# Kernel tuning notes

Measured on AMD Instinct MI355X. Metric: run time of the kernel, lower is better.

## Reference

```python
import jax, jax.numpy as jnp
import numpy as np

D_MODEL = 2048
N_HEADS = 16
HEAD_DIM = D_MODEL // N_HEADS
D_FF = 4 * D_MODEL
BATCH = 2
SEQ = 2048
LN_EPS = 1e-5


def setup_inputs() -> dict:
    key = jax.random.key(0)
    ks = jax.random.split(key, 12)
    s = 0.02
    return {
        "x": jax.random.normal(ks[0], (BATCH, SEQ, D_MODEL), dtype=jnp.float32),
        "alibi_bias": jax.random.normal(ks[1], (N_HEADS, SEQ, SEQ), dtype=jnp.float32),
        "W_q": jax.random.normal(ks[2], (D_MODEL, D_MODEL), dtype=jnp.float32) * s,
        "W_k": jax.random.normal(ks[3], (D_MODEL, D_MODEL), dtype=jnp.float32) * s,
        "W_v": jax.random.normal(ks[4], (D_MODEL, D_MODEL), dtype=jnp.float32) * s,
        "W_o": jax.random.normal(ks[5], (D_MODEL, D_MODEL), dtype=jnp.float32) * s,
        "ln1_g": jnp.ones((D_MODEL,), dtype=jnp.float32),
        "ln1_b": jnp.zeros((D_MODEL,), dtype=jnp.float32),
        "ln2_g": jnp.ones((D_MODEL,), dtype=jnp.float32),
        "ln2_b": jnp.zeros((D_MODEL,), dtype=jnp.float32),
        "ffn_w1": jax.random.normal(ks[6], (D_MODEL, D_FF), dtype=jnp.float32) * s,
        "ffn_b1": jnp.zeros((D_FF,), dtype=jnp.float32),
        "ffn_w2": jax.random.normal(ks[7], (D_FF, D_MODEL), dtype=jnp.float32) * s,
        "ffn_b2": jnp.zeros((D_MODEL,), dtype=jnp.float32),
    }


def _layernorm(x, g, b):
    mu = jnp.mean(x, axis=-1, keepdims=True)
    var = jnp.mean(jnp.square(x - mu), axis=-1, keepdims=True)
    return (x - mu) * jax.lax.rsqrt(var + LN_EPS) * g + b


def _mha(x, alibi_bias, W_q, W_k, W_v, W_o):
    B, S, _ = x.shape
    # nn.Linear applies x @ W.T; here W_* are stored as (in, out) so plain matmul.
    q = (x @ W_q).reshape(B, S, N_HEADS, HEAD_DIM).transpose(0, 2, 1, 3)
    k = (x @ W_k).reshape(B, S, N_HEADS, HEAD_DIM).transpose(0, 2, 1, 3)
    v = (x @ W_v).reshape(B, S, N_HEADS, HEAD_DIM).transpose(0, 2, 1, 3)
    q = q / np.sqrt(HEAD_DIM).astype(np.float32)
    scores = jnp.einsum("bhqd,bhkd->bhqk", q, k)  # [B,H,S,S]
    scores = scores + alibi_bias[None]
    causal = jnp.triu(jnp.ones((S, S), dtype=bool), k=1)
    scores = jnp.where(causal, jnp.finfo(scores.dtype).min, scores)
    attn = jax.nn.softmax(scores, axis=-1)
    out = jnp.einsum("bhqk,bhkd->bhqd", attn, v)
    out = out.transpose(0, 2, 1, 3).reshape(B, S, D_MODEL)
    return out @ W_o


def reference(x, alibi_bias, W_q, W_k, W_v, W_o, ln1_g, ln1_b, ln2_g, ln2_b,
              ffn_w1, ffn_b1, ffn_w2, ffn_b2):
    # Attention block (pre-LN, residual); dropout is identity in eval mode.
    h = x + _mha(_layernorm(x, ln1_g, ln1_b), alibi_bias, W_q, W_k, W_v, W_o)
    # FFN block
    n2 = _layernorm(h, ln2_g, ln2_b)
    ffn = jax.nn.gelu(n2 @ ffn_w1 + ffn_b1, approximate=False) @ ffn_w2 + ffn_b2
    return h + ffn
```

## Files before the change

### kernel.cpp

```cpp
#include <hip/hip_runtime.h>
#include <math.h>

#define DM   2048
#define DFF  8192
#define NH   16
#define HD   128
#define SEQ  2048
#define MROWS 4096

typedef __attribute__((ext_vector_type(4))) float  f32x4;
typedef __attribute__((ext_vector_type(8))) __bf16 bf16x8;
typedef __attribute__((ext_vector_type(4))) short  short4_t;

#define VMCNT(n) asm volatile("s_waitcnt vmcnt(" #n ")" ::: "memory")
#define LGKM0()  asm volatile("s_waitcnt lgkmcnt(0)" ::: "memory")
#define SBAR()   asm volatile("s_barrier" ::: "memory")
#define SCHEDB() __builtin_amdgcn_sched_barrier(0)

__device__ inline unsigned short f2bf(float f) {
  union { float f; unsigned int u; } x; x.f = f;
  unsigned int r = x.u + 0x7FFFu + ((x.u >> 16) & 1u);
  return (unsigned short)(r >> 16);
}

__device__ inline void gload16(const void* g, void* l) {
  __builtin_amdgcn_global_load_lds(
      (const __attribute__((address_space(1))) unsigned int*)g,
      (__attribute__((address_space(3))) unsigned int*)l, 16, 0, 0);
}

__global__ __launch_bounds__(256) void ln_kernel(
    const float* __restrict__ in, const float* __restrict__ gw,
    const float* __restrict__ bw, unsigned short* __restrict__ out)
{
  const int row = blockIdx.x;
  const float* xr = in + (size_t)row * DM;
  const int t = threadIdx.x, lane = t & 63, w = t >> 6;
  float4 v0 = ((const float4*)xr)[t];
  float4 v1 = ((const float4*)xr)[t + 256];
  float s = v0.x+v0.y+v0.z+v0.w + v1.x+v1.y+v1.z+v1.w;
  float s2 = v0.x*v0.x+v0.y*v0.y+v0.z*v0.z+v0.w*v0.w
           + v1.x*v1.x+v1.y*v1.y+v1.z*v1.z+v1.w*v1.w;
  #pragma unroll
  for (int off = 32; off; off >>= 1) { s += __shfl_xor(s, off); s2 += __shfl_xor(s2, off); }
  __shared__ float rs[4], rs2[4];
  if (lane == 0) { rs[w] = s; rs2[w] = s2; }
  __syncthreads();
  s = rs[0] + rs[1] + rs[2] + rs[3];
  s2 = rs2[0] + rs2[1] + rs2[2] + rs2[3];
  const float mu = s * (1.0f / DM);
  const float var = s2 * (1.0f / DM) - mu * mu;
  const float rstd = rsqrtf(var + 1e-5f);
  float4 g0 = ((const float4*)gw)[t],     b0 = ((const float4*)bw)[t];
  float4 g1 = ((const float4*)gw)[t+256], b1 = ((const float4*)bw)[t+256];
  unsigned short* o = out + (size_t)row * DM;
  int i0 = t * 4, i1 = (t + 256) * 4;
  o[i0+0] = f2bf((v0.x-mu)*rstd*g0.x + b0.x);
  o[i0+1] = f2bf((v0.y-mu)*rstd*g0.y + b0.y);
  o[i0+2] = f2bf((v0.z-mu)*rstd*g0.z + b0.z);
  o[i0+3] = f2bf((v0.w-mu)*rstd*g0.w + b0.w);
  o[i1+0] = f2bf((v1.x-mu)*rstd*g1.x + b1.x);
  o[i1+1] = f2bf((v1.y-mu)*rstd*g1.y + b1.y);
  o[i1+2] = f2bf((v1.z-mu)*rstd*g1.z + b1.z);
  o[i1+3] = f2bf((v1.w-mu)*rstd*g1.w + b1.w);
}

__global__ void transpose_kernel(const float* __restrict__ in,
                                 unsigned short* __restrict__ out,
                                 int nrows, int ncols)
{
  __shared__ float tile[32][33];
  const int bx = blockIdx.x * 32;
  const int by = blockIdx.y * 32;
  const int tx = threadIdx.x, ty = threadIdx.y;
  #pragma unroll
  for (int i = ty; i < 32; i += 8)
    tile[i][tx] = in[(size_t)(by + i) * ncols + bx + tx];
  __syncthreads();
  #pragma unroll
  for (int i = ty; i < 32; i += 8)
    out[(size_t)(bx + i) * nrows + by + tx] = f2bf(tile[tx][i]);
}

__global__ void transpose4_kernel(const float* __restrict__ w0,
                                  const float* __restrict__ w1,
                                  const float* __restrict__ w2,
                                  const float* __restrict__ w3,
                                  unsigned short* __restrict__ out)
{
  __shared__ float tile[32][33];
  const float* srcs[4] = {w0, w1, w2, w3};
  const float* in = srcs[blockIdx.z];
  unsigned short* o = out + (size_t)blockIdx.z * DM * DM;
  const int bx = blockIdx.x * 32;
  const int by = blockIdx.y * 32;
  const int tx = threadIdx.x, ty = threadIdx.y;
  #pragma unroll
  for (int i = ty; i < 32; i += 8)
    tile[i][tx] = in[(size_t)(by + i) * DM + bx + tx];
  __syncthreads();
  #pragma unroll
  for (int i = ty; i < 32; i += 8)
    o[(size_t)(bx + i) * DM + by + tx] = f2bf(tile[tx][i]);
}

enum { EP_QKV = 0, EP_WO = 3, EP_FFN1 = 4, EP_FFN2 = 5 };

template <int MODE>
__global__ __launch_bounds__(512, 2) void gemm_kernel(
    const unsigned short* __restrict__ A,
    const unsigned short* __restrict__ Bt,
    int K, int N,
    const float* __restrict__ res,
    const float* __restrict__ bias,
    void* __restrict__ out)
{
  __shared__ unsigned short lds[2][3][8192];

  const int t = threadIdx.x;
  const int w = t >> 6, lane = t & 63;
  const int wm = w >> 2, wn = w & 3;
  const int c = lane & 15, g = lane >> 4;
  const int l3 = lane >> 3, l7 = lane & 7;
  const int cs = c & 7;

  const long bm = (long)blockIdx.x * 128;
  const long bn = (long)blockIdx.y * 256;
  const int NT = K >> 6;
  const size_t Ksz = (size_t)K;

  const int scol = (l7 ^ l3) * 8;
  const int r0a = w * 16;

  auto stA = [&](int T) {
    unsigned short* d = &lds[T & 1][0][r0a * 64];
    #pragma unroll
    for (int j = 0; j < 2; j++)
      gload16(A + (bm + r0a + j * 8 + l3) * Ksz + T * 64 + scol, d + j * 512);
  };
  auto stB = [&](int T, int nh) {
    unsigned short* d = &lds[T & 1][1 + nh][r0a * 64];
    #pragma unroll
    for (int j = 0; j < 2; j++)
      gload16(Bt + (bn + nh * 128 + r0a + j * 8 + l3) * Ksz + T * 64 + scol, d + j * 512);
  };

  f32x4 acc[2][2][2][2];
  #pragma unroll
  for (int i = 0; i < 2; i++)
    #pragma unroll
    for (int jq = 0; jq < 2; jq++)
      #pragma unroll
      for (int m = 0; m < 2; m++)
        #pragma unroll
        for (int n = 0; n < 2; n++) acc[i][jq][m][n] = (f32x4){0.f, 0.f, 0.f, 0.f};

  stA(0); stB(0, 0); stB(0, 1);
  stA(1); stB(1, 0);
  VMCNT(4);
  SBAR();

  const int arow = (wm * 64 + c) * 64;
  const int brow = (wn * 32 + c) * 64;
  const int k0o = (g ^ cs) * 8;
  const int k1o = ((4 | g) ^ cs) * 8;

  for (int T = 0; T < NT; T++) {
    const unsigned short* LA  = lds[T & 1][0];
    const unsigned short* LB0 = lds[T & 1][1];
    const unsigned short* LB1 = lds[T & 1][2];
    bf16x8 a[2][2][2], b[2][2];

    #pragma unroll
    for (int mh = 0; mh < 2; mh++)
      #pragma unroll
      for (int m = 0; m < 2; m++) {
        a[mh][m][0] = *(const bf16x8*)&LA[arow + mh * 2048 + m * 1024 + k0o];
        a[mh][m][1] = *(const bf16x8*)&LA[arow + mh * 2048 + m * 1024 + k1o];
      }
    #pragma unroll
    for (int n = 0; n < 2; n++) {
      b[n][0] = *(const bf16x8*)&LB0[brow + n * 1024 + k0o];
      b[n][1] = *(const bf16x8*)&LB0[brow + n * 1024 + k1o];
    }
    if (T + 1 < NT) stB(T + 1, 1);
    SBAR();
    LGKM0(); SCHEDB();
    __builtin_amdgcn_s_setprio(1);
    #pragma unroll
    for (int kk = 0; kk < 2; kk++)
      #pragma unroll
      for (int mh = 0; mh < 2; mh++)
        #pragma unroll
        for (int m = 0; m < 2; m++)
          #pragma unroll
          for (int n = 0; n < 2; n++)
            acc[mh][0][m][n] = __builtin_amdgcn_mfma_f32_16x16x32_bf16(a[mh][m][kk], b[n][kk], acc[mh][0][m][n], 0, 0, 0);
    __builtin_amdgcn_s_setprio(0);
    SBAR();

    #pragma unroll
    for (int n = 0; n < 2; n++) {
      b[n][0] = *(const bf16x8*)&LB1[brow + n * 1024 + k0o];
      b[n][1] = *(const bf16x8*)&LB1[brow + n * 1024 + k1o];
    }
    if (T + 2 < NT) { stA(T + 2); stB(T + 2, 0); }
    SBAR();
    LGKM0(); SCHEDB();
    __builtin_amdgcn_s_setprio(1);
    #pragma unroll
    for (int kk = 0; kk < 2; kk++)
      #pragma unroll
      for (int mh = 0; mh < 2; mh++)
        #pragma unroll
        for (int m = 0; m < 2; m++)
          #pragma unroll
          for (int n = 0; n < 2; n++)
            acc[mh][1][m][n] = __builtin_amdgcn_mfma_f32_16x16x32_bf16(a[mh][m][kk], b[n][kk], acc[mh][1][m][n], 0, 0, 0);
    __builtin_amdgcn_s_setprio(0);
    if (T + 2 < NT) { VMCNT(4); } else { VMCNT(0); }
    SBAR();
  }

  #pragma unroll
  for (int mh = 0; mh < 2; mh++)
    #pragma unroll
    for (int nh = 0; nh < 2; nh++)
      #pragma unroll
      for (int m = 0; m < 2; m++)
        #pragma unroll
        for (int n = 0; n < 2; n++) {
          const long row0 = bm + wm * 64 + mh * 32 + m * 16 + g * 4;
          const long col  = bn + nh * 128 + wn * 32 + n * 16 + c;
          #pragma unroll
          for (int r = 0; r < 4; r++) {
            const long row = row0 + r;
            float v = acc[mh][nh][m][n][r];
            if constexpr (MODE == EP_QKV) {
              const int slot = (int)(col >> 11);
              const long cc = col & 2047;
              const long hh = cc >> 7, dd = cc & 127;
              const long bb = row >> 11, ss = row & 2047;
              unsigned short* o = (unsigned short*)out;
              if (slot == 0)
                o[((bb * NH + hh) * SEQ + ss) * HD + dd] = f2bf(v * 0.08838834764831845f);
              else if (slot == 1)
                o[8388608 + ((bb * NH + hh) * SEQ + ss) * HD + dd] = f2bf(v);
              else
                o[16777216 + ((bb * NH + hh) * HD + dd) * SEQ + ss] = f2bf(v);
            } else if constexpr (MODE == EP_WO) {
              ((float*)out)[row * DM + col] = res[row * DM + col] + v;
            } else if constexpr (MODE == EP_FFN1) {
              float u = v + bias[col];
              float y = 0.7978845608028654f * (u + 0.044715f * u * u * u);
              float e = __expf(-2.0f * fabsf(y));
              float th = (1.0f - e) / (1.0f + e);
              th = (y < 0.0f) ? -th : th;
              ((unsigned short*)out)[row * (long)N + col] = f2bf(0.5f * u * (1.0f + th));
            } else {
              ((float*)out)[row * DM + col] = res[row * DM + col] + v + bias[col];
            }
          }
        }
}

__global__ __launch_bounds__(256) void attn_kernel(
    const unsigned short* __restrict__ Q,
    const unsigned short* __restrict__ Kg,
    const unsigned short* __restrict__ Vt,
    const float* __restrict__ alibi,
    unsigned short* __restrict__ Out)
{
  __shared__ unsigned short lds[2][16384];

  const int bh = blockIdx.x;
  const int h = bh & (NH - 1);
  const int b = bh >> 4;
  const int j = blockIdx.y;
  const int t = threadIdx.x;
  const int w = t >> 6;
  const int lane = t & 63;
  const int c = lane & 15, g = lane >> 4;
  const int cx = (c & 7) << 4;

  const char* KpB = (const char*)(Kg + (size_t)bh * SEQ * HD);
  const char* VpB = (const char*)(Vt + (size_t)bh * SEQ * HD);
  const unsigned short* Qp = Q + (size_t)bh * SEQ * HD;
  const float* Ah = alibi + (size_t)h * SEQ * SEQ;

  #pragma unroll 1
  for (int half = 0; half < 2; half++) {
    const int cidx = half ? (31 - j) : j;
    const int nt = cidx + 1;
    const int qb = cidx * 64;
    const int q0 = qb + w * 16, qc = q0 + c;

    bf16x8 qf[4];
    #pragma unroll
    for (int dt = 0; dt < 4; dt++)
      qf[dt] = *(const bf16x8*)(Qp + (size_t)qc * HD + dt * 32 + g * 8);

    f32x4 oacc[8];
    #pragma unroll
    for (int d = 0; d < 8; d++) oacc[d] = (f32x4){0.f, 0.f, 0.f, 0.f};
    float m_run = -1e30f, s_run = 0.f;
    const float* Ap = Ah + (size_t)qc * SEQ;

    auto stage = [&](int tt, unsigned short* dst) {
      const size_t kvo = (size_t)tt * 64;
      #pragma unroll
      for (int k = 0; k < 8; k++) {
        const int o = w * 8192 + k * 1024 + lane * 16;
        if (w < 2) {
          const int so = o ^ (((o >> 8) & 7) << 4);
          gload16(KpB + kvo * 256 + so, dst + ((w * 8192 + k * 1024) >> 1));
        } else {
          const int o2 = o - 16384;
          const int d = o2 >> 7, win = o2 & 127;
          gload16(VpB + (size_t)d * 4096 + kvo * 2 + (win ^ ((d & 7) << 4)),
                  dst + ((w * 8192 + k * 1024) >> 1));
        }
      }
    };

    stage(0, lds[0]);
    __syncthreads();
    int buf = 0;

    for (int tt = 0; tt < nt; tt++) {
      if (tt + 1 < nt) stage(tt + 1, lds[buf ^ 1]);
      const unsigned short* LK = lds[buf];
      const unsigned short* LV = lds[buf] + 8192;
      const int kv0 = tt * 64;

      f32x4 sc[4];
      #pragma unroll
      for (int st = 0; st < 4; st++) sc[st] = (f32x4){0.f, 0.f, 0.f, 0.f};
      #pragma unroll
      for (int dt = 0; dt < 4; dt++)
        #pragma unroll
        for (int st = 0; st < 4; st++) {
          bf16x8 kf = *(const bf16x8*)&LK[(st * 4096 + c * 256 + ((dt * 64 + g * 16) ^ cx)) >> 1];
          sc[st] = __builtin_amdgcn_mfma_f32_16x16x32_bf16(kf, qf[dt], sc[st], 0, 0, 0);
        }

      float4 al[4];
      #pragma unroll
      for (int st = 0; st < 4; st++) al[st] = *(const float4*)(Ap + kv0 + st * 16 + g * 4);
      float scr[16];
      #pragma unroll
      for (int st = 0; st < 4; st++) {
        scr[st*4+0] = (kv0 + st*16 + g*4 + 0 > qc) ? -1e30f : sc[st][0] + al[st].x;
        scr[st*4+1] = (kv0 + st*16 + g*4 + 1 > qc) ? -1e30f : sc[st][1] + al[st].y;
        scr[st*4+2] = (kv0 + st*16 + g*4 + 2 > qc) ? -1e30f : sc[st][2] + al[st].z;
        scr[st*4+3] = (kv0 + st*16 + g*4 + 3 > qc) ? -1e30f : sc[st][3] + al[st].w;
      }

      float tm = scr[0];
      #pragma unroll
      for (int i = 1; i < 16; i++) tm = fmaxf(tm, scr[i]);
      tm = fmaxf(tm, __shfl_xor(tm, 16));
      tm = fmaxf(tm, __shfl_xor(tm, 32));
      const float m_new = fmaxf(m_run, tm);
      const float corr = __expf(m_run - m_new);
      float pv[16]; float ps = 0.f;
      #pragma unroll
      for (int i = 0; i < 16; i++) { pv[i] = __expf(scr[i] - m_new); ps += pv[i]; }
      ps += __shfl_xor(ps, 16);
      ps += __shfl_xor(ps, 32);
      s_run = s_run * corr + ps;
      m_run = m_new;

      short4_t pf[4];
      #pragma unroll
      for (int st = 0; st < 4; st++) {
        pf[st][0] = (short)f2bf(pv[st*4+0]); pf[st][1] = (short)f2bf(pv[st*4+1]);
        pf[st][2] = (short)f2bf(pv[st*4+2]); pf[st][3] = (short)f2bf(pv[st*4+3]);
      }

      float cf[4];
      #pragma unroll
      for (int r = 0; r < 4; r++) cf[r] = __shfl(corr, g * 4 + r);

      #pragma unroll
      for (int dt = 0; dt < 8; dt++) {
        f32x4 o = oacc[dt];
        o[0] *= cf[0]; o[1] *= cf[1]; o[2] *= cf[2]; o[3] *= cf[3];
        #pragma unroll
        for (int st = 0; st < 4; st++) {
          short4_t vf = *(const short4_t*)&LV[((dt * 16 + c) * 128 + ((st * 32 + g * 8) ^ cx)) >> 1];
          o = __builtin_amdgcn_mfma_f32_16x16x16bf16_1k(pf[st], vf, o, 0, 0, 0);
        }
        oacc[dt] = o;
      }

      __syncthreads();
      buf ^= 1;
    }

    float inv[4];
    #pragma unroll
    for (int r = 0; r < 4; r++) inv[r] = 1.0f / __shfl(s_run, g * 4 + r);
    #pragma unroll
    for (int dt = 0; dt < 8; dt++)
      #pragma unroll
      for (int r = 0; r < 4; r++)
        Out[(size_t)(b * SEQ + q0 + g * 4 + r) * DM + h * HD + dt * 16 + c] =
            f2bf(oacc[dt][r] * inv[r]);
  }
}

extern "C" void kernel_launch(void* const* d_in, const int* in_sizes, int n_in,
                              void* d_out, int out_size, void* d_ws, size_t ws_size,
                              hipStream_t stream) {
  const float* x     = (const float*)d_in[0];
  const float* alibi = (const float*)d_in[1];
  const float* Wq    = (const float*)d_in[2];
  const float* Wk    = (const float*)d_in[3];
  const float* Wv    = (const float*)d_in[4];
  const float* Wo    = (const float*)d_in[5];
  const float* ln1g  = (const float*)d_in[6];
  const float* ln1b  = (const float*)d_in[7];
  const float* ln2g  = (const float*)d_in[8];
  const float* ln2b  = (const float*)d_in[9];
  const float* w1    = (const float*)d_in[10];
  const float* b1    = (const float*)d_in[11];
  const float* w2    = (const float*)d_in[12];
  const float* b2    = (const float*)d_in[13];

  char* ws = (char*)d_ws;
  float*          hbuf = (float*)(ws);
  unsigned short* xn   = (unsigned short*)(ws + (32ull  << 20));
  unsigned short* qb   = (unsigned short*)(ws + (48ull  << 20));
  unsigned short* kb   = (unsigned short*)(ws + (64ull  << 20));
  unsigned short* vt   = (unsigned short*)(ws + (80ull  << 20));
  unsigned short* ao   = (unsigned short*)(ws + (96ull  << 20));
  unsigned short* wt   = (unsigned short*)(ws + (112ull << 20));
  unsigned short* a1   = (unsigned short*)(ws + (48ull  << 20));

  dim3 blk256(256);
  dim3 blk512(512);
  dim3 tb(32, 8);

  ln_kernel<<<MROWS, blk256, 0, stream>>>(x, ln1g, ln1b, xn);

  transpose4_kernel<<<dim3(DM/32, DM/32, 4), tb, 0, stream>>>(Wq, Wk, Wv, Wo, wt);

  gemm_kernel<EP_QKV><<<dim3(MROWS/128, (3*DM)/256), blk512, 0, stream>>>(
      xn, wt, DM, 3*DM, nullptr, nullptr, qb);

  attn_kernel<<<dim3(NH * 2, 16), blk256, 0, stream>>>(qb, kb, vt, alibi, ao);

  gemm_kernel<EP_WO><<<dim3(MROWS/128, DM/256), blk512, 0, stream>>>(
      ao, wt + 3ull * DM * DM, DM, DM, x, nullptr, hbuf);

  ln_kernel<<<MROWS, blk256, 0, stream>>>(hbuf, ln2g, ln2b, xn);

  transpose_kernel<<<dim3(DFF/32, DM/32), tb, 0, stream>>>(w1, wt, DM, DFF);
  gemm_kernel<EP_FFN1><<<dim3(MROWS/128, DFF/256), blk512, 0, stream>>>(xn, wt, DM, DFF, nullptr, b1, a1);

  transpose_kernel<<<dim3(DM/32, DFF/32), tb, 0, stream>>>(w2, wt, DFF, DM);
  gemm_kernel<EP_FFN2><<<dim3(MROWS/128, DM/256), blk512, 0, stream>>>(a1, wt, DFF, DM, hbuf, b2, (float*)d_out);
}
```

Baseline: 703.4 us.

## Enlarge GEMM tiles to 256x256 and split-K the Wo and FFN2 GEMMs with atomics

The GEMM block tile grows from 128x256 to 256x256, giving each warp 128x64 outputs and more register reuse per LDS load, with a four-phase pipelined k-loop. The narrow Wo and FFN2 GEMMs use split-K over two z-slices, accumulating with float atomicAdd into buffers pre-seeded with the residual (memcpy of x) or residual plus bias (a new ln2 kernel writes h+b2 into the output). This is meant to keep enough blocks in flight once tiles get larger and to fold the residual epilogues away. The cost is atomic traffic, a nondeterministic summation order, and higher register and LDS pressure at the launch bound of two blocks.

```diff
diff --git a/kernel.cpp b/kernel.cpp
--- a/kernel.cpp
+++ b/kernel.cpp
@@ -65,6 +65,50 @@
   o[i1+3] = f2bf((v1.w-mu)*rstd*g1.w + b1.w);
 }
 
+__global__ __launch_bounds__(256) void ln2_kernel(
+    const float* __restrict__ in, const float* __restrict__ gw,
+    const float* __restrict__ bw, unsigned short* __restrict__ out,
+    float* __restrict__ pre, const float* __restrict__ bias2)
+{
+  const int row = blockIdx.x;
+  const float* xr = in + (size_t)row * DM;
+  const int t = threadIdx.x, lane = t & 63, w = t >> 6;
+  float4 v0 = ((const float4*)xr)[t];
+  float4 v1 = ((const float4*)xr)[t + 256];
+  float s = v0.x+v0.y+v0.z+v0.w + v1.x+v1.y+v1.z+v1.w;
+  float s2 = v0.x*v0.x+v0.y*v0.y+v0.z*v0.z+v0.w*v0.w
+           + v1.x*v1.x+v1.y*v1.y+v1.z*v1.z+v1.w*v1.w;
+  #pragma unroll
+  for (int off = 32; off; off >>= 1) { s += __shfl_xor(s, off); s2 += __shfl_xor(s2, off); }
+  __shared__ float rs[4], rs2[4];
+  if (lane == 0) { rs[w] = s; rs2[w] = s2; }
+  __syncthreads();
+  s = rs[0] + rs[1] + rs[2] + rs[3];
+  s2 = rs2[0] + rs2[1] + rs2[2] + rs2[3];
+  const float mu = s * (1.0f / DM);
+  const float var = s2 * (1.0f / DM) - mu * mu;
+  const float rstd = rsqrtf(var + 1e-5f);
+  float4 g0 = ((const float4*)gw)[t],     b0 = ((const float4*)bw)[t];
+  float4 g1 = ((const float4*)gw)[t+256], b1 = ((const float4*)bw)[t+256];
+  float4 q0 = ((const float4*)bias2)[t], q1 = ((const float4*)bias2)[t+256];
+  unsigned short* o = out + (size_t)row * DM;
+  float* pr = pre + (size_t)row * DM;
+  int i0 = t * 4, i1 = (t + 256) * 4;
+  o[i0+0] = f2bf((v0.x-mu)*rstd*g0.x + b0.x);
+  o[i0+1] = f2bf((v0.y-mu)*rstd*g0.y + b0.y);
+  o[i0+2] = f2bf((v0.z-mu)*rstd*g0.z + b0.z);
+  o[i0+3] = f2bf((v0.w-mu)*rstd*g0.w + b0.w);
+  o[i1+0] = f2bf((v1.x-mu)*rstd*g1.x + b1.x);
+  o[i1+1] = f2bf((v1.y-mu)*rstd*g1.y + b1.y);
+  o[i1+2] = f2bf((v1.z-mu)*rstd*g1.z + b1.z);
+  o[i1+3] = f2bf((v1.w-mu)*rstd*g1.w + b1.w);
+  float4 p0, p1;
+  p0.x = v0.x + q0.x; p0.y = v0.y + q0.y; p0.z = v0.z + q0.z; p0.w = v0.w + q0.w;
+  p1.x = v1.x + q1.x; p1.y = v1.y + q1.y; p1.z = v1.z + q1.z; p1.w = v1.w + q1.w;
+  ((float4*)pr)[t] = p0;
+  ((float4*)pr)[t + 256] = p1;
+}
+
 __global__ void transpose_kernel(const float* __restrict__ in,
                                  unsigned short* __restrict__ out,
                                  int nrows, int ncols)
@@ -104,164 +148,178 @@
     o[(size_t)(bx + i) * DM + by + tx] = f2bf(tile[tx][i]);
 }
 
-enum { EP_QKV = 0, EP_WO = 3, EP_FFN1 = 4, EP_FFN2 = 5 };
+enum { EP_QKV = 0, EP_FFN1 = 1, EP_ATOMIC = 2 };
 
 template <int MODE>
 __global__ __launch_bounds__(512, 2) void gemm_kernel(
     const unsigned short* __restrict__ A,
     const unsigned short* __restrict__ Bt,
-    int K, int N,
-    const float* __restrict__ res,
+    int K, int kstride, int N,
     const float* __restrict__ bias,
     void* __restrict__ out)
 {
-  __shared__ unsigned short lds[2][3][8192];
+  __shared__ unsigned short lds[2][32768];
 
   const int t = threadIdx.x;
   const int w = t >> 6, lane = t & 63;
   const int wm = w >> 2, wn = w & 3;
   const int c = lane & 15, g = lane >> 4;
-  const int l3 = lane >> 3, l7 = lane & 7;
-  const int cs = c & 7;
-
-  const long bm = (long)blockIdx.x * 128;
+
+  const long bm = (long)blockIdx.x * 256;
   const long bn = (long)blockIdx.y * 256;
+  const long koff = (long)blockIdx.z * K;
   const int NT = K >> 6;
-  const size_t Ksz = (size_t)K;
-
-  const int scol = (l7 ^ l3) * 8;
-  const int r0a = w * 16;
-
-  auto stA = [&](int T) {
-    unsigned short* d = &lds[T & 1][0][r0a * 64];
-    #pragma unroll
-    for (int j = 0; j < 2; j++)
-      gload16(A + (bm + r0a + j * 8 + l3) * Ksz + T * 64 + scol, d + j * 512);
+  const size_t ks = (size_t)kstride;
+
+  const int tr  = t >> 3;
+  const int tc8 = (t & 7) * 8;
+  const int sch = ((t & 7) ^ (tr & 7)) * 8;
+
+  auto stageA = [&](int T, int mh) {
+    const int s = T & 1;
+    const int r0 = mh * 64 + tr;
+    gload16(A + (bm + r0) * ks + koff + T * 64 + sch,       &lds[s][r0 * 64 + tc8]);
+    gload16(A + (bm + r0 + 128) * ks + koff + T * 64 + sch, &lds[s][(r0 + 128) * 64 + tc8]);
   };
-  auto stB = [&](int T, int nh) {
-    unsigned short* d = &lds[T & 1][1 + nh][r0a * 64];
-    #pragma unroll
-    for (int j = 0; j < 2; j++)
-      gload16(Bt + (bn + nh * 128 + r0a + j * 8 + l3) * Ksz + T * 64 + scol, d + j * 512);
+  auto stageB = [&](int T, int nh) {
+    const int s = T & 1;
+    const int r0 = nh * 32 + (tr & 31) + (tr >> 5) * 64;
+    gload16(Bt + (bn + r0) * ks + koff + T * 64 + sch,       &lds[s][16384 + r0 * 64 + tc8]);
+    gload16(Bt + (bn + r0 + 128) * ks + koff + T * 64 + sch, &lds[s][16384 + (r0 + 128) * 64 + tc8]);
   };
 
-  f32x4 acc[2][2][2][2];
-  #pragma unroll
-  for (int i = 0; i < 2; i++)
-    #pragma unroll
-    for (int jq = 0; jq < 2; jq++)
-      #pragma unroll
-      for (int m = 0; m < 2; m++)
-        #pragma unroll
-        for (int n = 0; n < 2; n++) acc[i][jq][m][n] = (f32x4){0.f, 0.f, 0.f, 0.f};
-
-  stA(0); stB(0, 0); stB(0, 1);
-  stA(1); stB(1, 0);
-  VMCNT(4);
+  f32x4 acc[8][4];
+  #pragma unroll
+  for (int i = 0; i < 8; i++)
+    #pragma unroll
+    for (int j = 0; j < 4; j++) acc[i][j] = (f32x4){0.f, 0.f, 0.f, 0.f};
+
+  const int xo0 = ((0 + g) ^ (c & 7)) * 8;
+  const int xo1 = ((4 + g) ^ (c & 7)) * 8;
+  const int abase = (wm * 128 + c) * 64;
+  const int bbase = 16384 + (wn * 64 + c) * 64;
+
+  stageA(0, 0); stageB(0, 0); stageA(0, 1); stageB(0, 1);
+  stageA(1, 0); stageB(1, 0); stageA(1, 1);
+  VMCNT(6);
   SBAR();
 
-  const int arow = (wm * 64 + c) * 64;
-  const int brow = (wn * 32 + c) * 64;
-  const int k0o = (g ^ cs) * 8;
-  const int k1o = ((4 | g) ^ cs) * 8;
+  bf16x8 a[4][2], b0[2][2], b1[2][2];
 
   for (int T = 0; T < NT; T++) {
-    const unsigned short* LA  = lds[T & 1][0];
-    const unsigned short* LB0 = lds[T & 1][1];
-    const unsigned short* LB1 = lds[T & 1][2];
-    bf16x8 a[2][2][2], b[2][2];
-
-    #pragma unroll
-    for (int mh = 0; mh < 2; mh++)
-      #pragma unroll
-      for (int m = 0; m < 2; m++) {
-        a[mh][m][0] = *(const bf16x8*)&LA[arow + mh * 2048 + m * 1024 + k0o];
-        a[mh][m][1] = *(const bf16x8*)&LA[arow + mh * 2048 + m * 1024 + k1o];
-      }
-    #pragma unroll
-    for (int n = 0; n < 2; n++) {
-      b[n][0] = *(const bf16x8*)&LB0[brow + n * 1024 + k0o];
-      b[n][1] = *(const bf16x8*)&LB0[brow + n * 1024 + k1o];
+    const unsigned short* Ls = lds[T & 1];
+
+    #pragma unroll
+    for (int mf = 0; mf < 4; mf++) {
+      a[mf][0] = *(const bf16x8*)&Ls[abase + mf * 1024 + xo0];
+      a[mf][1] = *(const bf16x8*)&Ls[abase + mf * 1024 + xo1];
     }
-    if (T + 1 < NT) stB(T + 1, 1);
+    #pragma unroll
+    for (int nf = 0; nf < 2; nf++) {
+      b0[nf][0] = *(const bf16x8*)&Ls[bbase + nf * 1024 + xo0];
+      b0[nf][1] = *(const bf16x8*)&Ls[bbase + nf * 1024 + xo1];
+    }
+    if (T + 1 < NT) stageB(T + 1, 1);
     SBAR();
     LGKM0(); SCHEDB();
     __builtin_amdgcn_s_setprio(1);
     #pragma unroll
     for (int kk = 0; kk < 2; kk++)
       #pragma unroll
-      for (int mh = 0; mh < 2; mh++)
+      for (int mf = 0; mf < 4; mf++)
         #pragma unroll
-        for (int m = 0; m < 2; m++)
-          #pragma unroll
-          for (int n = 0; n < 2; n++)
-            acc[mh][0][m][n] = __builtin_amdgcn_mfma_f32_16x16x32_bf16(a[mh][m][kk], b[n][kk], acc[mh][0][m][n], 0, 0, 0);
+        for (int nf = 0; nf < 2; nf++)
+          acc[mf][nf] = __builtin_amdgcn_mfma_f32_16x16x32_bf16(a[mf][kk], b0[nf][kk], acc[mf][nf], 0, 0, 0);
     __builtin_amdgcn_s_setprio(0);
     SBAR();
 
     #pragma unroll
-    for (int n = 0; n < 2; n++) {
-      b[n][0] = *(const bf16x8*)&LB1[brow + n * 1024 + k0o];
-      b[n][1] = *(const bf16x8*)&LB1[brow + n * 1024 + k1o];
+    for (int nf = 0; nf < 2; nf++) {
+      b1[nf][0] = *(const bf16x8*)&Ls[bbase + 2048 + nf * 1024 + xo0];
+      b1[nf][1] = *(const bf16x8*)&Ls[bbase + 2048 + nf * 1024 + xo1];
     }
-    if (T + 2 < NT) { stA(T + 2); stB(T + 2, 0); }
+    if (T + 2 < NT) stageA(T + 2, 0);
     SBAR();
     LGKM0(); SCHEDB();
     __builtin_amdgcn_s_setprio(1);
     #pragma unroll
     for (int kk = 0; kk < 2; kk++)
       #pragma unroll
-      for (int mh = 0; mh < 2; mh++)
+      for (int mf = 0; mf < 4; mf++)
         #pragma unroll
-        for (int m = 0; m < 2; m++)
-          #pragma unroll
-          for (int n = 0; n < 2; n++)
-            acc[mh][1][m][n] = __builtin_amdgcn_mfma_f32_16x16x32_bf16(a[mh][m][kk], b[n][kk], acc[mh][1][m][n], 0, 0, 0);
+        for (int nf = 0; nf < 2; nf++)
+          acc[mf][2 + nf] = __builtin_amdgcn_mfma_f32_16x16x32_bf16(a[mf][kk], b1[nf][kk], acc[mf][2 + nf], 0, 0, 0);
     __builtin_amdgcn_s_setprio(0);
-    if (T + 2 < NT) { VMCNT(4); } else { VMCNT(0); }
+    SBAR();
+
+    #pragma unroll
+    for (int mf = 0; mf < 4; mf++) {
+      a[mf][0] = *(const bf16x8*)&Ls[abase + 4096 + mf * 1024 + xo0];
+      a[mf][1] = *(const bf16x8*)&Ls[abase + 4096 + mf * 1024 + xo1];
+    }
+    if (T + 2 < NT) stageB(T + 2, 0);
+    SBAR();
+    LGKM0(); SCHEDB();
+    __builtin_amdgcn_s_setprio(1);
+    #pragma unroll
+    for (int kk = 0; kk < 2; kk++)
+      #pragma unroll
+      for (int mf = 0; mf < 4; mf++)
+        #pragma unroll
+        for (int nf = 0; nf < 2; nf++)
+          acc[4 + mf][nf] = __builtin_amdgcn_mfma_f32_16x16x32_bf16(a[mf][kk], b0[nf][kk], acc[4 + mf][nf], 0, 0, 0);
+    __builtin_amdgcn_s_setprio(0);
+    SBAR();
+
+    if (T + 2 < NT) stageA(T + 2, 1);
+    __builtin_amdgcn_s_setprio(1);
+    #pragma unroll
+    for (int kk = 0; kk < 2; kk++)
+      #pragma unroll
+      for (int mf = 0; mf < 4; mf++)
+        #pragma unroll
+        for (int nf = 0; nf < 2; nf++)
+          acc[4 + mf][2 + nf] = __builtin_amdgcn_mfma_f32_16x16x32_bf16(a[mf][kk], b1[nf][kk], acc[4 + mf][2 + nf], 0, 0, 0);
+    __builtin_amdgcn_s_setprio(0);
+    if (T + 2 < NT) { VMCNT(6); } else { VMCNT(0); }
     SBAR();
   }
 
   #pragma unroll
-  for (int mh = 0; mh < 2; mh++)
-    #pragma unroll
-    for (int nh = 0; nh < 2; nh++)
-      #pragma unroll
-      for (int m = 0; m < 2; m++)
-        #pragma unroll
-        for (int n = 0; n < 2; n++) {
-          const long row0 = bm + wm * 64 + mh * 32 + m * 16 + g * 4;
-          const long col  = bn + nh * 128 + wn * 32 + n * 16 + c;
-          #pragma unroll
-          for (int r = 0; r < 4; r++) {
-            const long row = row0 + r;
-            float v = acc[mh][nh][m][n][r];
-            if constexpr (MODE == EP_QKV) {
-              const int slot = (int)(col >> 11);
-              const long cc = col & 2047;
-              const long hh = cc >> 7, dd = cc & 127;
-              const long bb = row >> 11, ss = row & 2047;
-              unsigned short* o = (unsigned short*)out;
-              if (slot == 0)
-                o[((bb * NH + hh) * SEQ + ss) * HD + dd] = f2bf(v * 0.08838834764831845f);
-              else if (slot == 1)
-                o[8388608 + ((bb * NH + hh) * SEQ + ss) * HD + dd] = f2bf(v);
-              else
-                o[16777216 + ((bb * NH + hh) * HD + dd) * SEQ + ss] = f2bf(v);
-            } else if constexpr (MODE == EP_WO) {
-              ((float*)out)[row * DM + col] = res[row * DM + col] + v;
-            } else if constexpr (MODE == EP_FFN1) {
-              float u = v + bias[col];
-              float y = 0.7978845608028654f * (u + 0.044715f * u * u * u);
-              float e = __expf(-2.0f * fabsf(y));
-              float th = (1.0f - e) / (1.0f + e);
-              th = (y < 0.0f) ? -th : th;
-              ((unsigned short*)out)[row * (long)N + col] = f2bf(0.5f * u * (1.0f + th));
-            } else {
-              ((float*)out)[row * DM + col] = res[row * DM + col] + v + bias[col];
-            }
-          }
+  for (int mf = 0; mf < 8; mf++) {
+    const long row0 = bm + wm * 128 + mf * 16 + g * 4;
+    #pragma unroll
+    for (int nf = 0; nf < 4; nf++) {
+      const long col = bn + wn * 64 + nf * 16 + c;
+      #pragma unroll
+      for (int r = 0; r < 4; r++) {
+        const long row = row0 + r;
+        float v = acc[mf][nf][r];
+        if constexpr (MODE == EP_QKV) {
+          const int slot = (int)(col >> 11);
+          const long cc = col & 2047;
+          const long hh = cc >> 7, dd = cc & 127;
+          const long bb = row >> 11, ss = row & 2047;
+          unsigned short* o = (unsigned short*)out;
+          if (slot == 0)
+            o[((bb * NH + hh) * SEQ + ss) * HD + dd] = f2bf(v * 0.08838834764831845f);
+          else if (slot == 1)
+            o[8388608 + ((bb * NH + hh) * SEQ + ss) * HD + dd] = f2bf(v);
+          else
+            o[16777216 + ((bb * NH + hh) * HD + dd) * SEQ + ss] = f2bf(v);
+        } else if constexpr (MODE == EP_FFN1) {
+          float u = v + bias[col];
+          float y = 0.7978845608028654f * (u + 0.044715f * u * u * u);
+          float e = __expf(-2.0f * fabsf(y));
+          float th = (1.0f - e) / (1.0f + e);
+          th = (y < 0.0f) ? -th : th;
+          ((unsigned short*)out)[row * (long)N + col] = f2bf(0.5f * u * (1.0f + th));
+        } else {
+          atomicAdd(&((float*)out)[row * (long)N + col], v);
         }
+      }
+    }
+  }
 }
 
 __global__ __launch_bounds__(256) void attn_kernel(
@@ -443,22 +501,24 @@
   dim3 tb(32, 8);
 
   ln_kernel<<<MROWS, blk256, 0, stream>>>(x, ln1g, ln1b, xn);
-
   transpose4_kernel<<<dim3(DM/32, DM/32, 4), tb, 0, stream>>>(Wq, Wk, Wv, Wo, wt);
 
-  gemm_kernel<EP_QKV><<<dim3(MROWS/128, (3*DM)/256), blk512, 0, stream>>>(
-      xn, wt, DM, 3*DM, nullptr, nullptr, qb);
+  gemm_kernel<EP_QKV><<<dim3(MROWS/256, (3*DM)/256, 1), blk512, 0, stream>>>(
+      xn, wt, DM, DM, 3*DM, nullptr, qb);
 
   attn_kernel<<<dim3(NH * 2, 16), blk256, 0, stream>>>(qb, kb, vt, alibi, ao);
 
-  gemm_kernel<EP_WO><<<dim3(MROWS/128, DM/256), blk512, 0, stream>>>(
-      ao, wt + 3ull * DM * DM, DM, DM, x, nullptr, hbuf);
-
-  ln_kernel<<<MROWS, blk256, 0, stream>>>(hbuf, ln2g, ln2b, xn);
+  hipMemcpyAsync(hbuf, x, (size_t)MROWS * DM * 4, hipMemcpyDeviceToDevice, stream);
+  gemm_kernel<EP_ATOMIC><<<dim3(MROWS/256, DM/256, 2), blk512, 0, stream>>>(
+      ao, wt + 3ull * DM * DM, DM/2, DM, DM, nullptr, hbuf);
+
+  ln2_kernel<<<MROWS, blk256, 0, stream>>>(hbuf, ln2g, ln2b, xn, (float*)d_out, b2);
 
   transpose_kernel<<<dim3(DFF/32, DM/32), tb, 0, stream>>>(w1, wt, DM, DFF);
-  gemm_kernel<EP_FFN1><<<dim3(MROWS/128, DFF/256), blk512, 0, stream>>>(xn, wt, DM, DFF, nullptr, b1, a1);
+  gemm_kernel<EP_FFN1><<<dim3(MROWS/256, DFF/256, 1), blk512, 0, stream>>>(
+      xn, wt, DM, DM, DFF, b1, a1);
 
   transpose_kernel<<<dim3(DM/32, DFF/32), tb, 0, stream>>>(w2, wt, DFF, DM);
-  gemm_kernel<EP_FFN2><<<dim3(MROWS/128, DM/256), blk512, 0, stream>>>(a1, wt, DFF, DM, hbuf, b2, (float*)d_out);
-}
+  gemm_kernel<EP_ATOMIC><<<dim3(MROWS/256, DM/256, 2), blk512, 0, stream>>>(
+      a1, wt, DFF/2, DFF, DM, nullptr, (float*)d_out);
+}
```

After: 760.5 us. 1.08x slower.

## Add 256x256-tile GEMM kernel for QKV and FFN1 projections

Applied to the files above, without the earlier changes.

Adds a new GEMM kernel with 256x256 output tiles, 128 KB of double-buffered LDS and a four-phase pipeline that interleaves MFMA quadrants with staging of the next K tile. It is used for the wide-N QKV and FFN1 projections. The original 128x256 kernel is kept for the Wo and FFN2 GEMMs. The LDS wait in both kernels is also moved from before each MFMA block to after it. Larger tiles raise arithmetic intensity and cut global traffic per FLOP, at the cost of more accumulator registers, lower occupancy, and fewer blocks for the QKV grid.

```diff
diff --git a/kernel.cpp b/kernel.cpp
--- a/kernel.cpp
+++ b/kernel.cpp
@@ -15,7 +15,6 @@
 #define VMCNT(n) asm volatile("s_waitcnt vmcnt(" #n ")" ::: "memory")
 #define LGKM0()  asm volatile("s_waitcnt lgkmcnt(0)" ::: "memory")
 #define SBAR()   asm volatile("s_barrier" ::: "memory")
-#define SCHEDB() __builtin_amdgcn_sched_barrier(0)
 
 __device__ inline unsigned short f2bf(float f) {
   union { float f; unsigned int u; } x; x.f = f;
@@ -104,10 +103,181 @@
     o[(size_t)(bx + i) * DM + by + tx] = f2bf(tile[tx][i]);
 }
 
-enum { EP_QKV = 0, EP_WO = 3, EP_FFN1 = 4, EP_FFN2 = 5 };
+enum { EPA_QKV = 0, EPA_FFN1 = 1 };
 
 template <int MODE>
-__global__ __launch_bounds__(512, 2) void gemm_kernel(
+__global__ __launch_bounds__(512, 2) void gemm256_kernel(
+    const unsigned short* __restrict__ A,
+    const unsigned short* __restrict__ Bt,
+    int K, int N,
+    const float* __restrict__ bias,
+    void* __restrict__ out)
+{
+  __shared__ unsigned short lds[2][32768];
+
+  const int t = threadIdx.x;
+  const int w = t >> 6, lane = t & 63;
+  const int wm = w >> 2, wn = w & 3;
+  const int c = lane & 15, g = lane >> 4;
+
+  const long bm = (long)blockIdx.x * 256;
+  const long bn = (long)blockIdx.y * 256;
+  const int NT = K >> 6;
+  const size_t ks = (size_t)K;
+
+  const int tr  = t >> 3;
+  const int tc8 = (t & 7) * 8;
+  const int sch = ((t & 7) ^ (tr & 7)) * 8;
+
+  auto stageA = [&](int T, int mh) {
+    const int s = T & 1;
+    const int r0 = mh * 64 + tr;
+    gload16(A + (bm + r0) * ks + T * 64 + sch,       &lds[s][r0 * 64 + tc8]);
+    gload16(A + (bm + r0 + 128) * ks + T * 64 + sch, &lds[s][(r0 + 128) * 64 + tc8]);
+  };
+  auto stageB = [&](int T, int nh) {
+    const int s = T & 1;
+    const int r0 = nh * 32 + (tr & 31) + (tr >> 5) * 64;
+    gload16(Bt + (bn + r0) * ks + T * 64 + sch,       &lds[s][16384 + r0 * 64 + tc8]);
+    gload16(Bt + (bn + r0 + 128) * ks + T * 64 + sch, &lds[s][16384 + (r0 + 128) * 64 + tc8]);
+  };
+
+  f32x4 acc[8][4];
+  #pragma unroll
+  for (int i = 0; i < 8; i++)
+    #pragma unroll
+    for (int j = 0; j < 4; j++) acc[i][j] = (f32x4){0.f, 0.f, 0.f, 0.f};
+
+  const int xo0 = ((0 + g) ^ (c & 7)) * 8;
+  const int xo1 = ((4 + g) ^ (c & 7)) * 8;
+  const int abase = (wm * 128 + c) * 64;
+  const int bbase = 16384 + (wn * 64 + c) * 64;
+
+  stageA(0, 0); stageB(0, 0); stageA(0, 1); stageB(0, 1);
+  stageA(1, 0); stageB(1, 0); stageA(1, 1);
+  VMCNT(6);
+  SBAR();
+
+  bf16x8 a[4][2], b0[2][2], b1[2][2];
+
+  for (int T = 0; T < NT; T++) {
+    const unsigned short* Ls = lds[T & 1];
+
+    #pragma unroll
+    for (int mf = 0; mf < 4; mf++) {
+      a[mf][0] = *(const bf16x8*)&Ls[abase + mf * 1024 + xo0];
+      a[mf][1] = *(const bf16x8*)&Ls[abase + mf * 1024 + xo1];
+    }
+    #pragma unroll
+    for (int nf = 0; nf < 2; nf++) {
+      b0[nf][0] = *(const bf16x8*)&Ls[bbase + nf * 1024 + xo0];
+      b0[nf][1] = *(const bf16x8*)&Ls[bbase + nf * 1024 + xo1];
+    }
+    if (T + 1 < NT) stageB(T + 1, 1);
+    SBAR();
+    __builtin_amdgcn_s_setprio(1);
+    #pragma unroll
+    for (int kk = 0; kk < 2; kk++)
+      #pragma unroll
+      for (int mf = 0; mf < 4; mf++)
+        #pragma unroll
+        for (int nf = 0; nf < 2; nf++)
+          acc[mf][nf] = __builtin_amdgcn_mfma_f32_16x16x32_bf16(a[mf][kk], b0[nf][kk], acc[mf][nf], 0, 0, 0);
+    __builtin_amdgcn_s_setprio(0);
+    LGKM0();
+    SBAR();
+
+    #pragma unroll
+    for (int nf = 0; nf < 2; nf++) {
+      b1[nf][0] = *(const bf16x8*)&Ls[bbase + 2048 + nf * 1024 + xo0];
+      b1[nf][1] = *(const bf16x8*)&Ls[bbase + 2048 + nf * 1024 + xo1];
+    }
+    if (T + 2 < NT) stageA(T + 2, 0);
+    SBAR();
+    __builtin_amdgcn_s_setprio(1);
+    #pragma unroll
+    for (int kk = 0; kk < 2; kk++)
+      #pragma unroll
+      for (int mf = 0; mf < 4; mf++)
+        #pragma unroll
+        for (int nf = 0; nf < 2; nf++)
+          acc[mf][2 + nf] = __builtin_amdgcn_mfma_f32_16x16x32_bf16(a[mf][kk], b1[nf][kk], acc[mf][2 + nf], 0, 0, 0);
+    __builtin_amdgcn_s_setprio(0);
+    LGKM0();
+    SBAR();
+
+    #pragma unroll
+    for (int mf = 0; mf < 4; mf++) {
+      a[mf][0] = *(const bf16x8*)&Ls[abase + 4096 + mf * 1024 + xo0];
+      a[mf][1] = *(const bf16x8*)&Ls[abase + 4096 + mf * 1024 + xo1];
+    }
+    if (T + 2 < NT) stageB(T + 2, 0);
+    SBAR();
+    __builtin_amdgcn_s_setprio(1);
+    #pragma unroll
+    for (int kk = 0; kk < 2; kk++)
+      #pragma unroll
+      for (int mf = 0; mf < 4; mf++)
+        #pragma unroll
+        for (int nf = 0; nf < 2; nf++)
+          acc[4 + mf][nf] = __builtin_amdgcn_mfma_f32_16x16x32_bf16(a[mf][kk], b0[nf][kk], acc[4 + mf][nf], 0, 0, 0);
+    __builtin_amdgcn_s_setprio(0);
+    LGKM0();
+    SBAR();
+
+    if (T + 2 < NT) stageA(T + 2, 1);
+    __builtin_amdgcn_s_setprio(1);
+    #pragma unroll
+    for (int kk = 0; kk < 2; kk++)
+      #pragma unroll
+      for (int mf = 0; mf < 4; mf++)
+        #pragma unroll
+        for (int nf = 0; nf < 2; nf++)
+          acc[4 + mf][2 + nf] = __builtin_amdgcn_mfma_f32_16x16x32_bf16(a[mf][kk], b1[nf][kk], acc[4 + mf][2 + nf], 0, 0, 0);
+    __builtin_amdgcn_s_setprio(0);
+    if (T + 2 < NT) { VMCNT(6); } else { VMCNT(0); }
+    SBAR();
+  }
+
+  #pragma unroll
+  for (int mf = 0; mf < 8; mf++) {
+    const long row0 = bm + wm * 128 + mf * 16 + g * 4;
+    #pragma unroll
+    for (int nf = 0; nf < 4; nf++) {
+      const long col = bn + wn * 64 + nf * 16 + c;
+      #pragma unroll
+      for (int r = 0; r < 4; r++) {
+        const long row = row0 + r;
+        float v = acc[mf][nf][r];
+        if constexpr (MODE == EPA_QKV) {
+          const int slot = (int)(col >> 11);
+          const long cc = col & 2047;
+          const long hh = cc >> 7, dd = cc & 127;
+          const long bb = row >> 11, ss = row & 2047;
+          unsigned short* o = (unsigned short*)out;
+          if (slot == 0)
+            o[((bb * NH + hh) * SEQ + ss) * HD + dd] = f2bf(v * 0.08838834764831845f);
+          else if (slot == 1)
+            o[8388608 + ((bb * NH + hh) * SEQ + ss) * HD + dd] = f2bf(v);
+          else
+            o[16777216 + ((bb * NH + hh) * HD + dd) * SEQ + ss] = f2bf(v);
+        } else {
+          float u = v + bias[col];
+          float y = 0.7978845608028654f * (u + 0.044715f * u * u * u);
+          float e = __expf(-2.0f * fabsf(y));
+          float th = (1.0f - e) / (1.0f + e);
+          th = (y < 0.0f) ? -th : th;
+          ((unsigned short*)out)[row * (long)N + col] = f2bf(0.5f * u * (1.0f + th));
+        }
+      }
+    }
+  }
+}
+
+enum { EPB_WO = 0, EPB_FFN2 = 1 };
+
+template <int MODE>
+__global__ __launch_bounds__(512, 2) void gemm128_kernel(
     const unsigned short* __restrict__ A,
     const unsigned short* __restrict__ Bt,
     int K, int N,
@@ -122,7 +292,6 @@
   const int wm = w >> 2, wn = w & 3;
   const int c = lane & 15, g = lane >> 4;
   const int l3 = lane >> 3, l7 = lane & 7;
-  const int cs = c & 7;
 
   const long bm = (long)blockIdx.x * 128;
   const long bn = (long)blockIdx.y * 256;
@@ -162,8 +331,8 @@
 
   const int arow = (wm * 64 + c) * 64;
   const int brow = (wn * 32 + c) * 64;
-  const int k0o = (g ^ cs) * 8;
-  const int k1o = ((4 | g) ^ cs) * 8;
+  const int k0o = (g ^ (c & 7)) * 8;
+  const int k1o = ((4 | g) ^ (c & 7)) * 8;
 
   for (int T = 0; T < NT; T++) {
     const unsigned short* LA  = lds[T & 1][0];
@@ -185,7 +354,6 @@
     }
     if (T + 1 < NT) stB(T + 1, 1);
     SBAR();
-    LGKM0(); SCHEDB();
     __builtin_amdgcn_s_setprio(1);
     #pragma unroll
     for (int kk = 0; kk < 2; kk++)
@@ -197,6 +365,7 @@
           for (int n = 0; n < 2; n++)
             acc[mh][0][m][n] = __builtin_amdgcn_mfma_f32_16x16x32_bf16(a[mh][m][kk], b[n][kk], acc[mh][0][m][n], 0, 0, 0);
     __builtin_amdgcn_s_setprio(0);
+    LGKM0();
     SBAR();
 
     #pragma unroll
@@ -206,7 +375,6 @@
     }
     if (T + 2 < NT) { stA(T + 2); stB(T + 2, 0); }
     SBAR();
-    LGKM0(); SCHEDB();
     __builtin_amdgcn_s_setprio(1);
     #pragma unroll
     for (int kk = 0; kk < 2; kk++)
@@ -218,6 +386,7 @@
           for (int n = 0; n < 2; n++)
             acc[mh][1][m][n] = __builtin_amdgcn_mfma_f32_16x16x32_bf16(a[mh][m][kk], b[n][kk], acc[mh][1][m][n], 0, 0, 0);
     __builtin_amdgcn_s_setprio(0);
+    LGKM0();
     if (T + 2 < NT) { VMCNT(4); } else { VMCNT(0); }
     SBAR();
   }
@@ -236,27 +405,8 @@
           for (int r = 0; r < 4; r++) {
             const long row = row0 + r;
             float v = acc[mh][nh][m][n][r];
-            if constexpr (MODE == EP_QKV) {
-              const int slot = (int)(col >> 11);
-              const long cc = col & 2047;
-              const long hh = cc >> 7, dd = cc & 127;
-              const long bb = row >> 11, ss = row & 2047;
-              unsigned short* o = (unsigned short*)out;
-              if (slot == 0)
-                o[((bb * NH + hh) * SEQ + ss) * HD + dd] = f2bf(v * 0.08838834764831845f);
-              else if (slot == 1)
-                o[8388608 + ((bb * NH + hh) * SEQ + ss) * HD + dd] = f2bf(v);
-              else
-                o[16777216 + ((bb * NH + hh) * HD + dd) * SEQ + ss] = f2bf(v);
-            } else if constexpr (MODE == EP_WO) {
+            if constexpr (MODE == EPB_WO) {
               ((float*)out)[row * DM + col] = res[row * DM + col] + v;
-            } else if constexpr (MODE == EP_FFN1) {
-              float u = v + bias[col];
-              float y = 0.7978845608028654f * (u + 0.044715f * u * u * u);
-              float e = __expf(-2.0f * fabsf(y));
-              float th = (1.0f - e) / (1.0f + e);
-              th = (y < 0.0f) ? -th : th;
-              ((unsigned short*)out)[row * (long)N + col] = f2bf(0.5f * u * (1.0f + th));
             } else {
               ((float*)out)[row * DM + col] = res[row * DM + col] + v + bias[col];
             }
@@ -443,22 +593,23 @@
   dim3 tb(32, 8);
 
   ln_kernel<<<MROWS, blk256, 0, stream>>>(x, ln1g, ln1b, xn);
-
   transpose4_kernel<<<dim3(DM/32, DM/32, 4), tb, 0, stream>>>(Wq, Wk, Wv, Wo, wt);
 
-  gemm_kernel<EP_QKV><<<dim3(MROWS/128, (3*DM)/256), blk512, 0, stream>>>(
-      xn, wt, DM, 3*DM, nullptr, nullptr, qb);
+  gemm256_kernel<EPA_QKV><<<dim3(MROWS/256, (3*DM)/256), blk512, 0, stream>>>(
+      xn, wt, DM, 3*DM, nullptr, qb);
 
   attn_kernel<<<dim3(NH * 2, 16), blk256, 0, stream>>>(qb, kb, vt, alibi, ao);
 
-  gemm_kernel<EP_WO><<<dim3(MROWS/128, DM/256), blk512, 0, stream>>>(
+  gemm128_kernel<EPB_WO><<<dim3(MROWS/128, DM/256), blk512, 0, stream>>>(
       ao, wt + 3ull * DM * DM, DM, DM, x, nullptr, hbuf);
 
   ln_kernel<<<MROWS, blk256, 0, stream>>>(hbuf, ln2g, ln2b, xn);
 
   transpose_kernel<<<dim3(DFF/32, DM/32), tb, 0, stream>>>(w1, wt, DM, DFF);
-  gemm_kernel<EP_FFN1><<<dim3(MROWS/128, DFF/256), blk512, 0, stream>>>(xn, wt, DM, DFF, nullptr, b1, a1);
+  gemm256_kernel<EPA_FFN1><<<dim3(MROWS/256, DFF/256), blk512, 0, stream>>>(
+      xn, wt, DM, DFF, b1, a1);
 
   transpose_kernel<<<dim3(DM/32, DFF/32), tb, 0, stream>>>(w2, wt, DFF, DM);
-  gemm_kernel<EP_FFN2><<<dim3(MROWS/128, DM/256), blk512, 0, stream>>>(a1, wt, DFF, DM, hbuf, b2, (float*)d_out);
-}
+  gemm128_kernel<EPB_FFN2><<<dim3(MROWS/128, DM/256), blk512, 0, stream>>>(
+      a1, wt, DFF, DM, hbuf, b2, (float*)d_out);
+}
```

Result: no change. 698.7 us (-0.7%).
